# Kernel tuning notes

Measured on AMD Instinct MI355X. Metric: run time of the kernel, lower is better.

## Reference

```python
import jax, jax.numpy as jnp
import numpy as np

ROUTER_AUX_LOSS_COEF = 0.001


def setup_inputs() -> dict:
    key = jax.random.key(0)
    k1, k2, k3, k4 = jax.random.split(key, 4)
    B, S, H = 2, 2048, 2048
    E, I = 8, 768
    return {
        "hidden_states": jax.random.normal(k1, (B, S, H), dtype=jnp.float32),
        "gate_w": jax.random.normal(k2, (H, E), dtype=jnp.float32) * 0.02,
        "gate_up_proj": jax.random.normal(k3, (E, 2 * I, H), dtype=jnp.float32) * 0.02,
        "down_proj": jax.random.normal(k4, (E, H, I), dtype=jnp.float32) * 0.02,
        "num_experts_per_tok": 2,
    }


def reference(hidden_states, gate_w, gate_up_proj, down_proj, num_experts_per_tok):
    B, S, H = hidden_states.shape
    E = gate_w.shape[1]
    x = hidden_states.reshape(-1, H)  # (T, H)
    T = x.shape[0]

    # Router
    router_logits = x @ gate_w  # (T, E)
    routing_weights = jax.nn.softmax(router_logits, axis=-1)
    topk_w, selected = jax.lax.top_k(routing_weights, num_experts_per_tok)  # (T, K)
    topk_w = topk_w / jnp.sum(topk_w, axis=-1, keepdims=True)  # norm_topk_prob

    # Dense (T, E) combine weights: zero for non-selected experts. Identical math
    # to gathering per-token expert weights, but avoids materializing (T,K,2I,H).
    w_dense = jnp.zeros((T, E), x.dtype).at[jnp.arange(T)[:, None], selected].set(topk_w)

    # Expert GEMMs over all experts (non-selected contributions get weight 0)
    gate_up = jnp.einsum("th,efh->tef", x, gate_up_proj)  # (T, E, 2I)
    gate, up = jnp.split(gate_up, 2, axis=-1)
    inter = jax.nn.silu(gate) * up  # (T, E, I)
    expert_out = jnp.einsum("tei,ehi->teh", inter, down_proj)  # (T, E, H)
    final = jnp.einsum("teh,te->th", expert_out, w_dense).reshape(B, S, H)

    # Load-balancing auxiliary loss
    expert_probs = jnp.mean(routing_weights, axis=0)  # (E,)
    expert_mask = jax.nn.one_hot(selected, E, dtype=x.dtype)  # (T, K, E)
    expert_freq = jnp.mean(jnp.sum(expert_mask, axis=1), axis=0)  # (E,)
    aux_loss = jnp.sum(expert_probs * expert_freq) * E * ROUTER_AUX_LOSS_COEF

    return final, router_logits, aux_loss
```

## Files before the change

kernel.cpp:

```cpp
#include <hip/hip_runtime.h>
#include <hip/hip_bf16.h>
#include <math.h>

#define TT 4096
#define HH 2048
#define EE 8
#define II 768
#define TWOI 1536

typedef __attribute__((ext_vector_type(8))) short bf16v8;
typedef __attribute__((ext_vector_type(4))) float f32x4;

static __device__ __forceinline__ unsigned short f2bf(float f) {
    unsigned int u = __float_as_uint(f);
    unsigned int r = (u + 0x7fffu + ((u >> 16) & 1u)) >> 16;
    return (unsigned short)r;
}
static __device__ __forceinline__ float bf2f(unsigned short b) {
    return __uint_as_float(((unsigned int)b) << 16);
}
static __device__ __forceinline__ void cvt8(const float4 v0, const float4 v1,
                                            uint4& hi, uint4& lo) {
    float f[8] = {v0.x, v0.y, v0.z, v0.w, v1.x, v1.y, v1.z, v1.w};
    unsigned short h[8], l[8];
#pragma unroll
    for (int i = 0; i < 8; ++i) {
        h[i] = f2bf(f[i]);
        l[i] = f2bf(f[i] - bf2f(h[i]));
    }
    hi = make_uint4((unsigned)h[0] | ((unsigned)h[1] << 16),
                    (unsigned)h[2] | ((unsigned)h[3] << 16),
                    (unsigned)h[4] | ((unsigned)h[5] << 16),
                    (unsigned)h[6] | ((unsigned)h[7] << 16));
    lo = make_uint4((unsigned)l[0] | ((unsigned)l[1] << 16),
                    (unsigned)l[2] | ((unsigned)l[3] << 16),
                    (unsigned)l[4] | ((unsigned)l[5] << 16),
                    (unsigned)l[6] | ((unsigned)l[7] << 16));
}

__global__ __launch_bounds__(256) void router_kernel(
    const float* __restrict__ x, const float* __restrict__ gw,
    float* __restrict__ logits_out, int* __restrict__ counts,
    int* __restrict__ bucket_tok, float* __restrict__ bucket_w)
{
    const int wave = threadIdx.x >> 6;
    const int lane = threadIdx.x & 63;
    const int t = blockIdx.x * 4 + wave;

    float acc[EE];
#pragma unroll
    for (int e = 0; e < EE; ++e) acc[e] = 0.f;

    const float4* xr = (const float4*)(x + (size_t)t * HH);
    for (int i = lane; i < HH / 4; i += 64) {
        const float4 v = xr[i];
        const float* g = gw + (size_t)(i * 4) * EE;
#pragma unroll
        for (int e = 0; e < EE; ++e)
            acc[e] += v.x * g[e] + v.y * g[e + EE]
                    + v.z * g[e + 2 * EE] + v.w * g[e + 3 * EE];
    }
#pragma unroll
    for (int e = 0; e < EE; ++e) {
#pragma unroll
        for (int off = 32; off > 0; off >>= 1)
            acc[e] += __shfl_xor(acc[e], off, 64);
    }

    if (lane == 0) {
        float mx = acc[0];
#pragma unroll
        for (int e = 1; e < EE; ++e) mx = fmaxf(mx, acc[e]);
        float p[EE]; float s = 0.f;
#pragma unroll
        for (int e = 0; e < EE; ++e) { p[e] = expf(acc[e] - mx); s += p[e]; }
        const float inv = 1.f / s;
#pragma unroll
        for (int e = 0; e < EE; ++e) {
            p[e] *= inv;
            logits_out[(size_t)t * EE + e] = acc[e];
        }
        int i0 = 0;
#pragma unroll
        for (int e = 1; e < EE; ++e) if (p[e] > p[i0]) i0 = e;
        int i1 = (i0 == 0) ? 1 : 0;
#pragma unroll
        for (int e = 0; e < EE; ++e) if (e != i0 && p[e] > p[i1]) i1 = e;
        const float denom = 1.f / (p[i0] + p[i1]);
        const float w0 = p[i0] * denom, w1 = p[i1] * denom;
        int pos0 = atomicAdd(&counts[i0], 1);
        bucket_tok[i0 * TT + pos0] = t; bucket_w[i0 * TT + pos0] = w0;
        int pos1 = atomicAdd(&counts[i1], 1);
        bucket_tok[i1 * TT + pos1] = t; bucket_w[i1 * TT + pos1] = w1;
    }
}

__global__ __launch_bounds__(256) void finalize_router(
    const float* __restrict__ logits, const int* __restrict__ counts,
    int* __restrict__ offsets, float* __restrict__ aux_out)
{
    __shared__ float sums[EE];
    if (threadIdx.x < EE) sums[threadIdx.x] = 0.f;
    __syncthreads();
    float loc[EE];
#pragma unroll
    for (int e = 0; e < EE; ++e) loc[e] = 0.f;
    for (int t = threadIdx.x; t < TT; t += 256) {
        const float* lr = logits + (size_t)t * EE;
        float l[EE]; float mx = -1e30f;
#pragma unroll
        for (int e = 0; e < EE; ++e) { l[e] = lr[e]; mx = fmaxf(mx, l[e]); }
        float s = 0.f, p[EE];
#pragma unroll
        for (int e = 0; e < EE; ++e) { p[e] = expf(l[e] - mx); s += p[e]; }
        const float inv = 1.f / s;
#pragma unroll
        for (int e = 0; e < EE; ++e) loc[e] += p[e] * inv;
    }
#pragma unroll
    for (int e = 0; e < EE; ++e) atomicAdd(&sums[e], loc[e]);
    __syncthreads();
    if (threadIdx.x == 0) {
        int o = 0; float aux = 0.f;
        for (int e = 0; e < EE; ++e) {
            offsets[e] = o; o += counts[e];
            aux += (sums[e] / (float)TT) * ((float)counts[e] / (float)TT);
        }
        aux_out[0] = aux * (float)EE * 0.001f;
    }
}

#define AHI 0
#define ALO 8192
#define BHI 16384
#define BLO 24576

__global__ __launch_bounds__(256, 2) void moe_gateup(
    const float* __restrict__ x, const float* __restrict__ Wgu,
    const int* __restrict__ counts, const int* __restrict__ offsets,
    const int* __restrict__ bucket_tok, float* __restrict__ inter)
{
    const int bid = blockIdx.x;
    const int e = bid & 7;
    const int rem = bid >> 3;
    const int mb = rem / 12, nb = rem % 12;

    const int cnt = counts[e];
    const int m0 = mb * 128;
    if (m0 >= cnt) return;
    const int n0 = nb * 64;
    const int base = offsets[e];

    __shared__ unsigned char smem[32768];

    const int tid = threadIdx.x;
    const int lane = tid & 63;
    const int wid = tid >> 6;
    const int wm = wid >> 1, wn = wid & 1;

    const int srow = tid >> 1;
    const int sseg = tid & 1;
    const int arow = m0 + srow;
    const int atok = (arow < cnt) ? bucket_tok[e * TT + arow] : 0;
    const float* ag = x + (size_t)atok * HH + sseg * 16;
    const int bblk = srow >> 5, bc = srow & 31;
    const int bj = ((bblk & 1) ? II : 0) + n0 + ((bblk >> 1) << 5) + bc;
    const float* bg = Wgu + ((size_t)e * TWOI + bj) * HH + sseg * 16;
    const int au0 = srow * 64 + (((sseg << 1) | 0) ^ (srow & 3)) * 16;
    const int au1 = srow * 64 + (((sseg << 1) | 1) ^ (srow & 3)) * 16;

    int aoff[4], boff[4];
#pragma unroll
    for (int i = 0; i < 4; ++i) {
        int ra = wm * 64 + i * 16 + (lane & 15);
        aoff[i] = ra * 64 + (((lane >> 4) ^ (ra & 3)) * 16);
        int rb = wn * 64 + i * 16 + (lane & 15);
        boff[i] = rb * 64 + (((lane >> 4) ^ (rb & 3)) * 16);
    }

    f32x4 acc[4][4];
#pragma unroll
    for (int i = 0; i < 4; ++i)
#pragma unroll
        for (int j = 0; j < 4; ++j) acc[i][j] = f32x4{0.f, 0.f, 0.f, 0.f};

    float4 pa0 = *(const float4*)(ag + 0), pa1 = *(const float4*)(ag + 4);
    float4 pa2 = *(const float4*)(ag + 8), pa3 = *(const float4*)(ag + 12);
    float4 pb0 = *(const float4*)(bg + 0), pb1 = *(const float4*)(bg + 4);
    float4 pb2 = *(const float4*)(bg + 8), pb3 = *(const float4*)(bg + 12);

    const int NS = HH / 32;
    for (int s = 0; s < NS; ++s) {
        __syncthreads();
        uint4 hi, lo;
        cvt8(pa0, pa1, hi, lo);
        *(uint4*)(smem + AHI + au0) = hi; *(uint4*)(smem + ALO + au0) = lo;
        cvt8(pa2, pa3, hi, lo);
        *(uint4*)(smem + AHI + au1) = hi; *(uint4*)(smem + ALO + au1) = lo;
        cvt8(pb0, pb1, hi, lo);
        *(uint4*)(smem + BHI + au0) = hi; *(uint4*)(smem + BLO + au0) = lo;
        cvt8(pb2, pb3, hi, lo);
        *(uint4*)(smem + BHI + au1) = hi; *(uint4*)(smem + BLO + au1) = lo;
        __syncthreads();
        if (s + 1 < NS) {
            const int k0 = (s + 1) * 32;
            pa0 = *(const float4*)(ag + k0); pa1 = *(const float4*)(ag + k0 + 4);
            pa2 = *(const float4*)(ag + k0 + 8); pa3 = *(const float4*)(ag + k0 + 12);
            pb0 = *(const float4*)(bg + k0); pb1 = *(const float4*)(bg + k0 + 4);
            pb2 = *(const float4*)(bg + k0 + 8); pb3 = *(const float4*)(bg + k0 + 12);
        }
        bf16v8 ah[4], al[4], bh[4], bl[4];
#pragma unroll
        for (int i = 0; i < 4; ++i) {
            ah[i] = *(const bf16v8*)(smem + AHI + aoff[i]);
            al[i] = *(const bf16v8*)(smem + ALO + aoff[i]);
            bh[i] = *(const bf16v8*)(smem + BHI + boff[i]);
            bl[i] = *(const bf16v8*)(smem + BLO + boff[i]);
        }
#pragma unroll
        for (int i = 0; i < 4; ++i)
#pragma unroll
            for (int j = 0; j < 4; ++j) {
                acc[i][j] = __builtin_amdgcn_mfma_f32_16x16x32_bf16(ah[i], bh[j], acc[i][j], 0, 0, 0);
                acc[i][j] = __builtin_amdgcn_mfma_f32_16x16x32_bf16(ah[i], bl[j], acc[i][j], 0, 0, 0);
                acc[i][j] = __builtin_amdgcn_mfma_f32_16x16x32_bf16(al[i], bh[j], acc[i][j], 0, 0, 0);
            }
    }

#pragma unroll
    for (int mi = 0; mi < 4; ++mi)
#pragma unroll
        for (int np = 0; np < 2; ++np) {
            const f32x4 g = acc[mi][np], u = acc[mi][np + 2];
            const int colp = n0 + wn * 32 + np * 16 + (lane & 15);
#pragma unroll
            for (int j = 0; j < 4; ++j) {
                const int r = m0 + wm * 64 + mi * 16 + ((lane >> 4) << 2) + j;
                if (r < cnt) {
                    const float gg = g[j];
                    const float sv = gg / (1.f + expf(-gg));
                    inter[(size_t)(base + r) * II + colp] = sv * u[j];
                }
            }
        }
}

__global__ __launch_bounds__(256, 2) void moe_down(
    const float* __restrict__ inter, const float* __restrict__ Wd,
    const int* __restrict__ counts, const int* __restrict__ offsets,
    const int* __restrict__ bucket_tok, const float* __restrict__ bucket_w,
    float* __restrict__ out)
{
    const int bid = blockIdx.x;
    const int e = bid & 7;
    const int rem = bid >> 3;
    const int mb = rem >> 4, nb = rem & 15;

    const int cnt = counts[e];
    const int m0 = mb * 128;
    if (m0 >= cnt) return;
    const int n0 = nb * 128;
    const int base = offsets[e];

    __shared__ unsigned char smem[32768];

    const int tid = threadIdx.x;
    const int lane = tid & 63;
    const int wid = tid >> 6;
    const int wm = wid >> 1, wn = wid & 1;

    const int srow = tid >> 1;
    const int sseg = tid & 1;
    const int arow = m0 + srow;
    const int asafe = (arow < cnt) ? arow : 0;
    const float* ag = inter + (size_t)(base + asafe) * II + sseg * 16;
    const float* bg = Wd + ((size_t)e * HH + n0 + srow) * II + sseg * 16;
    const int au0 = srow * 64 + (((sseg << 1) | 0) ^ (srow & 3)) * 16;
    const int au1 = srow * 64 + (((sseg << 1) | 1) ^ (srow & 3)) * 16;

    int aoff[4], boff[4];
#pragma unroll
    for (int i = 0; i < 4; ++i) {
        int ra = wm * 64 + i * 16 + (lane & 15);
        aoff[i] = ra * 64 + (((lane >> 4) ^ (ra & 3)) * 16);
        int rb = wn * 64 + i * 16 + (lane & 15);
        boff[i] = rb * 64 + (((lane >> 4) ^ (rb & 3)) * 16);
    }

    f32x4 acc[4][4];
#pragma unroll
    for (int i = 0; i < 4; ++i)
#pragma unroll
        for (int j = 0; j < 4; ++j) acc[i][j] = f32x4{0.f, 0.f, 0.f, 0.f};

    float4 pa0 = *(const float4*)(ag + 0), pa1 = *(const float4*)(ag + 4);
    float4 pa2 = *(const float4*)(ag + 8), pa3 = *(const float4*)(ag + 12);
    float4 pb0 = *(const float4*)(bg + 0), pb1 = *(const float4*)(bg + 4);
    float4 pb2 = *(const float4*)(bg + 8), pb3 = *(const float4*)(bg + 12);

    const int NS = II / 32;
    for (int s = 0; s < NS; ++s) {
        __syncthreads();
        uint4 hi, lo;
        cvt8(pa0, pa1, hi, lo);
        *(uint4*)(smem + AHI + au0) = hi; *(uint4*)(smem + ALO + au0) = lo;
        cvt8(pa2, pa3, hi, lo);
        *(uint4*)(smem + AHI + au1) = hi; *(uint4*)(smem + ALO + au1) = lo;
        cvt8(pb0, pb1, hi, lo);
        *(uint4*)(smem + BHI + au0) = hi; *(uint4*)(smem + BLO + au0) = lo;
        cvt8(pb2, pb3, hi, lo);
        *(uint4*)(smem + BHI + au1) = hi; *(uint4*)(smem + BLO + au1) = lo;
        __syncthreads();
        if (s + 1 < NS) {
            const int k0 = (s + 1) * 32;
            pa0 = *(const float4*)(ag + k0); pa1 = *(const float4*)(ag + k0 + 4);
            pa2 = *(const float4*)(ag + k0 + 8); pa3 = *(const float4*)(ag + k0 + 12);
            pb0 = *(const float4*)(bg + k0); pb1 = *(const float4*)(bg + k0 + 4);
            pb2 = *(const float4*)(bg + k0 + 8); pb3 = *(const float4*)(bg + k0 + 12);
        }
        bf16v8 ah[4], al[4], bh[4], bl[4];
#pragma unroll
        for (int i = 0; i < 4; ++i) {
            ah[i] = *(const bf16v8*)(smem + AHI + aoff[i]);
            al[i] = *(const bf16v8*)(smem + ALO + aoff[i]);
            bh[i] = *(const bf16v8*)(smem + BHI + boff[i]);
            bl[i] = *(const bf16v8*)(smem + BLO + boff[i]);
        }
#pragma unroll
        for (int i = 0; i < 4; ++i)
#pragma unroll
            for (int j = 0; j < 4; ++j) {
                acc[i][j] = __builtin_amdgcn_mfma_f32_16x16x32_bf16(ah[i], bh[j], acc[i][j], 0, 0, 0);
                acc[i][j] = __builtin_amdgcn_mfma_f32_16x16x32_bf16(ah[i], bl[j], acc[i][j], 0, 0, 0);
                acc[i][j] = __builtin_amdgcn_mfma_f32_16x16x32_bf16(al[i], bh[j], acc[i][j], 0, 0, 0);
            }
    }

#pragma unroll
    for (int mi = 0; mi < 4; ++mi) {
        int rtok[4]; float rw[4]; int rok[4];
#pragma unroll
        for (int j = 0; j < 4; ++j) {
            const int r = m0 + wm * 64 + mi * 16 + ((lane >> 4) << 2) + j;
            rok[j] = (r < cnt);
            rtok[j] = rok[j] ? bucket_tok[e * TT + r] : 0;
            rw[j] = rok[j] ? bucket_w[e * TT + r] : 0.f;
        }
#pragma unroll
        for (int ni = 0; ni < 4; ++ni) {
            const int col = n0 + wn * 64 + ni * 16 + (lane & 15);
#pragma unroll
            for (int j = 0; j < 4; ++j)
                if (rok[j])
                    atomicAdd(out + (size_t)rtok[j] * HH + col, rw[j] * acc[mi][ni][j]);
        }
    }
}

extern "C" void kernel_launch(void* const* d_in, const int* in_sizes, int n_in,
                              void* d_out, int out_size, void* d_ws, size_t ws_size,
                              hipStream_t stream)
{
    const float* x   = (const float*)d_in[0];
    const float* gw  = (const float*)d_in[1];
    const float* wgu = (const float*)d_in[2];
    const float* wd  = (const float*)d_in[3];

    float* out_final  = (float*)d_out;
    float* out_logits = out_final + (size_t)TT * HH;
    float* out_aux    = out_logits + (size_t)TT * EE;

    int*   counts     = (int*)d_ws;
    int*   offsets    = counts + 8;
    int*   bucket_tok = (int*)d_ws + 64;
    float* bucket_w   = (float*)d_ws + 64 + EE * TT;
    float* inter      = (float*)d_ws + 64 + 2 * EE * TT;

    hipMemsetAsync(d_ws, 0, 256, stream);
    hipMemsetAsync(d_out, 0, sizeof(float) * (size_t)TT * HH, stream);

    router_kernel<<<TT / 4, 256, 0, stream>>>(x, gw, out_logits, counts,
                                              bucket_tok, bucket_w);
    finalize_router<<<1, 256, 0, stream>>>(out_logits, counts, offsets, out_aux);
    moe_gateup<<<12 * 32 * EE, 256, 0, stream>>>(x, wgu, counts, offsets,
                                                 bucket_tok, inter);
    moe_down<<<16 * 32 * EE, 256, 0, stream>>>(inter, wd, counts, offsets,
                                               bucket_tok, bucket_w, out_final);
}
```

Measured before the change: 674.6 us.

## Pre-split operands into bf16 hi/lo buffers and widen GEMM K-tiles

Adds a pre-pass that converts the expert weights to bf16 hi/lo planes, and has the router emit split activations. The GEMM kernels then load pre-split data and use a 64-wide K tile with larger shared memory, instead of converting fp32 to bf16 pairs inside every tile. The intermediate activations are also stored as hi/lo bf16. This removes redundant per-block conversion work but adds a full weight conversion pass on every call and needs a large workspace; the old path is kept as a fallback.

Measured after the change: 1.348 ms. +99.8%, slower.

```diff
diff --git a/kernel.cpp b/kernel.cpp
--- a/kernel.cpp
+++ b/kernel.cpp
@@ -38,10 +38,28 @@
                     (unsigned)l[6] | ((unsigned)l[7] << 16));
 }
 
+__global__ __launch_bounds__(256) void cvt_split(
+    const float* __restrict__ src, unsigned short* __restrict__ hi,
+    unsigned short* __restrict__ lo, int n8)
+{
+    int i = blockIdx.x * 256 + threadIdx.x;
+    const int stride = gridDim.x * 256;
+    for (; i < n8; i += stride) {
+        const float4 a = ((const float4*)src)[2 * i];
+        const float4 b = ((const float4*)src)[2 * i + 1];
+        uint4 h, l;
+        cvt8(a, b, h, l);
+        ((uint4*)hi)[i] = h;
+        ((uint4*)lo)[i] = l;
+    }
+}
+
 __global__ __launch_bounds__(256) void router_kernel(
     const float* __restrict__ x, const float* __restrict__ gw,
     float* __restrict__ logits_out, int* __restrict__ counts,
-    int* __restrict__ bucket_tok, float* __restrict__ bucket_w)
+    int* __restrict__ bucket_tok, float* __restrict__ bucket_w,
+    unsigned short* __restrict__ xhi, unsigned short* __restrict__ xlo,
+    int do_split)
 {
     const int wave = threadIdx.x >> 6;
     const int lane = threadIdx.x & 63;
@@ -59,6 +77,20 @@
         for (int e = 0; e < EE; ++e)
             acc[e] += v.x * g[e] + v.y * g[e + EE]
                     + v.z * g[e + 2 * EE] + v.w * g[e + 3 * EE];
+        if (do_split) {
+            const unsigned short h0 = f2bf(v.x), h1 = f2bf(v.y),
+                                 h2 = f2bf(v.z), h3 = f2bf(v.w);
+            const unsigned short l0 = f2bf(v.x - bf2f(h0)),
+                                 l1 = f2bf(v.y - bf2f(h1)),
+                                 l2 = f2bf(v.z - bf2f(h2)),
+                                 l3 = f2bf(v.w - bf2f(h3));
+            *(uint2*)(xhi + (size_t)t * HH + i * 4) =
+                make_uint2((unsigned)h0 | ((unsigned)h1 << 16),
+                           (unsigned)h2 | ((unsigned)h3 << 16));
+            *(uint2*)(xlo + (size_t)t * HH + i * 4) =
+                make_uint2((unsigned)l0 | ((unsigned)l1 << 16),
+                           (unsigned)l2 | ((unsigned)l3 << 16));
+        }
     }
 #pragma unroll
     for (int e = 0; e < EE; ++e) {
@@ -131,14 +163,16 @@
 }
 
 #define AHI 0
-#define ALO 8192
-#define BHI 16384
-#define BLO 24576
-
-__global__ __launch_bounds__(256, 2) void moe_gateup(
-    const float* __restrict__ x, const float* __restrict__ Wgu,
+#define ALO 16384
+#define BHI 32768
+#define BLO 49152
+
+__global__ __launch_bounds__(256, 2) void moe_gateup_v2(
+    const unsigned short* __restrict__ xhi, const unsigned short* __restrict__ xlo,
+    const unsigned short* __restrict__ guhi, const unsigned short* __restrict__ gulo,
     const int* __restrict__ counts, const int* __restrict__ offsets,
-    const int* __restrict__ bucket_tok, float* __restrict__ inter)
+    const int* __restrict__ bucket_tok,
+    unsigned short* __restrict__ ihi, unsigned short* __restrict__ ilo)
 {
     const int bid = blockIdx.x;
     const int e = bid & 7;
@@ -151,13 +185,266 @@
     const int n0 = nb * 64;
     const int base = offsets[e];
 
-    __shared__ unsigned char smem[32768];
+    __shared__ unsigned char smem[65536];
 
     const int tid = threadIdx.x;
     const int lane = tid & 63;
     const int wid = tid >> 6;
     const int wm = wid >> 1, wn = wid & 1;
 
+    const int srow = tid >> 1;
+    const int sseg = tid & 1;
+    const int arow = m0 + srow;
+    const int atok = (arow < cnt) ? bucket_tok[e * TT + arow] : 0;
+    const size_t aoffg = (size_t)atok * HH + sseg * 32;
+    const int bblk = srow >> 5, bc = srow & 31;
+    const int bj = ((bblk & 1) ? II : 0) + n0 + ((bblk >> 1) << 5) + bc;
+    const size_t boffg = ((size_t)e * TWOI + bj) * HH + sseg * 32;
+
+    int wu[4];
+#pragma unroll
+    for (int j = 0; j < 4; ++j)
+        wu[j] = srow * 128 + ((((sseg << 2) | j) ^ (srow & 7)) << 4);
+
+    int aoff[2][4], boff[2][4];
+#pragma unroll
+    for (int ks = 0; ks < 2; ++ks)
+#pragma unroll
+        for (int i = 0; i < 4; ++i) {
+            const int ra = wm * 64 + i * 16 + (lane & 15);
+            aoff[ks][i] = ra * 128 + ((((ks << 2) | (lane >> 4)) ^ (ra & 7)) << 4);
+            const int rb = wn * 64 + i * 16 + (lane & 15);
+            boff[ks][i] = rb * 128 + ((((ks << 2) | (lane >> 4)) ^ (rb & 7)) << 4);
+        }
+
+    f32x4 acc[4][4];
+#pragma unroll
+    for (int i = 0; i < 4; ++i)
+#pragma unroll
+        for (int j = 0; j < 4; ++j) acc[i][j] = f32x4{0.f, 0.f, 0.f, 0.f};
+
+    uint4 pAh[4], pAl[4], pBh[4], pBl[4];
+#pragma unroll
+    for (int j = 0; j < 4; ++j) {
+        pAh[j] = *(const uint4*)(xhi + aoffg + j * 8);
+        pAl[j] = *(const uint4*)(xlo + aoffg + j * 8);
+        pBh[j] = *(const uint4*)(guhi + boffg + j * 8);
+        pBl[j] = *(const uint4*)(gulo + boffg + j * 8);
+    }
+
+    const int NS = HH / 64;
+    for (int s = 0; s < NS; ++s) {
+        __syncthreads();
+#pragma unroll
+        for (int j = 0; j < 4; ++j) {
+            *(uint4*)(smem + AHI + wu[j]) = pAh[j];
+            *(uint4*)(smem + ALO + wu[j]) = pAl[j];
+            *(uint4*)(smem + BHI + wu[j]) = pBh[j];
+            *(uint4*)(smem + BLO + wu[j]) = pBl[j];
+        }
+        __syncthreads();
+        if (s + 1 < NS) {
+            const int k0 = (s + 1) * 64;
+#pragma unroll
+            for (int j = 0; j < 4; ++j) {
+                pAh[j] = *(const uint4*)(xhi + aoffg + k0 + j * 8);
+                pAl[j] = *(const uint4*)(xlo + aoffg + k0 + j * 8);
+                pBh[j] = *(const uint4*)(guhi + boffg + k0 + j * 8);
+                pBl[j] = *(const uint4*)(gulo + boffg + k0 + j * 8);
+            }
+        }
+#pragma unroll
+        for (int ks = 0; ks < 2; ++ks) {
+            bf16v8 ah[4], al[4], bh[4], bl[4];
+#pragma unroll
+            for (int i = 0; i < 4; ++i) {
+                ah[i] = *(const bf16v8*)(smem + AHI + aoff[ks][i]);
+                al[i] = *(const bf16v8*)(smem + ALO + aoff[ks][i]);
+                bh[i] = *(const bf16v8*)(smem + BHI + boff[ks][i]);
+                bl[i] = *(const bf16v8*)(smem + BLO + boff[ks][i]);
+            }
+#pragma unroll
+            for (int i = 0; i < 4; ++i)
+#pragma unroll
+                for (int j = 0; j < 4; ++j) {
+                    acc[i][j] = __builtin_amdgcn_mfma_f32_16x16x32_bf16(ah[i], bh[j], acc[i][j], 0, 0, 0);
+                    acc[i][j] = __builtin_amdgcn_mfma_f32_16x16x32_bf16(ah[i], bl[j], acc[i][j], 0, 0, 0);
+                    acc[i][j] = __builtin_amdgcn_mfma_f32_16x16x32_bf16(al[i], bh[j], acc[i][j], 0, 0, 0);
+                }
+        }
+    }
+
+#pragma unroll
+    for (int mi = 0; mi < 4; ++mi)
+#pragma unroll
+        for (int np = 0; np < 2; ++np) {
+            const f32x4 g = acc[mi][np], u = acc[mi][np + 2];
+            const int colp = n0 + wn * 32 + np * 16 + (lane & 15);
+#pragma unroll
+            for (int j = 0; j < 4; ++j) {
+                const int r = m0 + wm * 64 + mi * 16 + ((lane >> 4) << 2) + j;
+                if (r < cnt) {
+                    const float gg = g[j];
+                    const float val = gg / (1.f + expf(-gg)) * u[j];
+                    const unsigned short h = f2bf(val);
+                    const unsigned short l = f2bf(val - bf2f(h));
+                    ihi[(size_t)(base + r) * II + colp] = h;
+                    ilo[(size_t)(base + r) * II + colp] = l;
+                }
+            }
+        }
+}
+
+__global__ __launch_bounds__(256, 2) void moe_down_v2(
+    const unsigned short* __restrict__ ihi, const unsigned short* __restrict__ ilo,
+    const unsigned short* __restrict__ wdhi, const unsigned short* __restrict__ wdlo,
+    const int* __restrict__ counts, const int* __restrict__ offsets,
+    const int* __restrict__ bucket_tok, const float* __restrict__ bucket_w,
+    float* __restrict__ out)
+{
+    const int bid = blockIdx.x;
+    const int e = bid & 7;
+    const int rem = bid >> 3;
+    const int mb = rem >> 4, nb = rem & 15;
+
+    const int cnt = counts[e];
+    const int m0 = mb * 128;
+    if (m0 >= cnt) return;
+    const int n0 = nb * 128;
+    const int base = offsets[e];
+
+    __shared__ unsigned char smem[65536];
+
+    const int tid = threadIdx.x;
+    const int lane = tid & 63;
+    const int wid = tid >> 6;
+    const int wm = wid >> 1, wn = wid & 1;
+
+    const int srow = tid >> 1;
+    const int sseg = tid & 1;
+    const int arow = m0 + srow;
+    const int asafe = (arow < cnt) ? arow : 0;
+    const size_t aoffg = (size_t)(base + asafe) * II + sseg * 32;
+    const size_t boffg = ((size_t)e * HH + n0 + srow) * II + sseg * 32;
+
+    int wu[4];
+#pragma unroll
+    for (int j = 0; j < 4; ++j)
+        wu[j] = srow * 128 + ((((sseg << 2) | j) ^ (srow & 7)) << 4);
+
+    int aoff[2][4], boff[2][4];
+#pragma unroll
+    for (int ks = 0; ks < 2; ++ks)
+#pragma unroll
+        for (int i = 0; i < 4; ++i) {
+            const int ra = wm * 64 + i * 16 + (lane & 15);
+            aoff[ks][i] = ra * 128 + ((((ks << 2) | (lane >> 4)) ^ (ra & 7)) << 4);
+            const int rb = wn * 64 + i * 16 + (lane & 15);
+            boff[ks][i] = rb * 128 + ((((ks << 2) | (lane >> 4)) ^ (rb & 7)) << 4);
+        }
+
+    f32x4 acc[4][4];
+#pragma unroll
+    for (int i = 0; i < 4; ++i)
+#pragma unroll
+        for (int j = 0; j < 4; ++j) acc[i][j] = f32x4{0.f, 0.f, 0.f, 0.f};
+
+    uint4 pAh[4], pAl[4], pBh[4], pBl[4];
+#pragma unroll
+    for (int j = 0; j < 4; ++j) {
+        pAh[j] = *(const uint4*)(ihi + aoffg + j * 8);
+        pAl[j] = *(const uint4*)(ilo + aoffg + j * 8);
+        pBh[j] = *(const uint4*)(wdhi + boffg + j * 8);
+        pBl[j] = *(const uint4*)(wdlo + boffg + j * 8);
+    }
+
+    const int NS = II / 64;
+    for (int s = 0; s < NS; ++s) {
+        __syncthreads();
+#pragma unroll
+        for (int j = 0; j < 4; ++j) {
+            *(uint4*)(smem + AHI + wu[j]) = pAh[j];
+            *(uint4*)(smem + ALO + wu[j]) = pAl[j];
+            *(uint4*)(smem + BHI + wu[j]) = pBh[j];
+            *(uint4*)(smem + BLO + wu[j]) = pBl[j];
+        }
+        __syncthreads();
+        if (s + 1 < NS) {
+            const int k0 = (s + 1) * 64;
+#pragma unroll
+            for (int j = 0; j < 4; ++j) {
+                pAh[j] = *(const uint4*)(ihi + aoffg + k0 + j * 8);
+                pAl[j] = *(const uint4*)(ilo + aoffg + k0 + j * 8);
+                pBh[j] = *(const uint4*)(wdhi + boffg + k0 + j * 8);
+                pBl[j] = *(const uint4*)(wdlo + boffg + k0 + j * 8);
+            }
+        }
+#pragma unroll
+        for (int ks = 0; ks < 2; ++ks) {
+            bf16v8 ah[4], al[4], bh[4], bl[4];
+#pragma unroll
+            for (int i = 0; i < 4; ++i) {
+                ah[i] = *(const bf16v8*)(smem + AHI + aoff[ks][i]);
+                al[i] = *(const bf16v8*)(smem + ALO + aoff[ks][i]);
+                bh[i] = *(const bf16v8*)(smem + BHI + boff[ks][i]);
+                bl[i] = *(const bf16v8*)(smem + BLO + boff[ks][i]);
+            }
+#pragma unroll
+            for (int i = 0; i < 4; ++i)
+#pragma unroll
+                for (int j = 0; j < 4; ++j) {
+                    acc[i][j] = __builtin_amdgcn_mfma_f32_16x16x32_bf16(ah[i], bh[j], acc[i][j], 0, 0, 0);
+                    acc[i][j] = __builtin_amdgcn_mfma_f32_16x16x32_bf16(ah[i], bl[j], acc[i][j], 0, 0, 0);
+                    acc[i][j] = __builtin_amdgcn_mfma_f32_16x16x32_bf16(al[i], bh[j], acc[i][j], 0, 0, 0);
+                }
+        }
+    }
+
+#pragma unroll
+    for (int mi = 0; mi < 4; ++mi) {
+        int rtok[4]; float rw[4]; int rok[4];
+#pragma unroll
+        for (int j = 0; j < 4; ++j) {
+            const int r = m0 + wm * 64 + mi * 16 + ((lane >> 4) << 2) + j;
+            rok[j] = (r < cnt);
+            rtok[j] = rok[j] ? bucket_tok[e * TT + r] : 0;
+            rw[j] = rok[j] ? bucket_w[e * TT + r] : 0.f;
+        }
+#pragma unroll
+        for (int ni = 0; ni < 4; ++ni) {
+            const int col = n0 + wn * 64 + ni * 16 + (lane & 15);
+#pragma unroll
+            for (int j = 0; j < 4; ++j)
+                if (rok[j])
+                    atomicAdd(out + (size_t)rtok[j] * HH + col, rw[j] * acc[mi][ni][j]);
+        }
+    }
+}
+
+#define AHI1 0
+#define ALO1 8192
+#define BHI1 16384
+#define BLO1 24576
+
+__global__ __launch_bounds__(256, 2) void moe_gateup_r4(
+    const float* __restrict__ x, const float* __restrict__ Wgu,
+    const int* __restrict__ counts, const int* __restrict__ offsets,
+    const int* __restrict__ bucket_tok, float* __restrict__ inter)
+{
+    const int bid = blockIdx.x;
+    const int e = bid & 7;
+    const int rem = bid >> 3;
+    const int mb = rem / 12, nb = rem % 12;
+    const int cnt = counts[e];
+    const int m0 = mb * 128;
+    if (m0 >= cnt) return;
+    const int n0 = nb * 64;
+    const int base = offsets[e];
+    __shared__ unsigned char smem[32768];
+    const int tid = threadIdx.x;
+    const int lane = tid & 63;
+    const int wid = tid >> 6;
+    const int wm = wid >> 1, wn = wid & 1;
     const int srow = tid >> 1;
     const int sseg = tid & 1;
     const int arow = m0 + srow;
@@ -168,7 +455,6 @@
     const float* bg = Wgu + ((size_t)e * TWOI + bj) * HH + sseg * 16;
     const int au0 = srow * 64 + (((sseg << 1) | 0) ^ (srow & 3)) * 16;
     const int au1 = srow * 64 + (((sseg << 1) | 1) ^ (srow & 3)) * 16;
-
     int aoff[4], boff[4];
 #pragma unroll
     for (int i = 0; i < 4; ++i) {
@@ -177,30 +463,27 @@
         int rb = wn * 64 + i * 16 + (lane & 15);
         boff[i] = rb * 64 + (((lane >> 4) ^ (rb & 3)) * 16);
     }
-
     f32x4 acc[4][4];
 #pragma unroll
     for (int i = 0; i < 4; ++i)
 #pragma unroll
         for (int j = 0; j < 4; ++j) acc[i][j] = f32x4{0.f, 0.f, 0.f, 0.f};
-
     float4 pa0 = *(const float4*)(ag + 0), pa1 = *(const float4*)(ag + 4);
     float4 pa2 = *(const float4*)(ag + 8), pa3 = *(const float4*)(ag + 12);
     float4 pb0 = *(const float4*)(bg + 0), pb1 = *(const float4*)(bg + 4);
     float4 pb2 = *(const float4*)(bg + 8), pb3 = *(const float4*)(bg + 12);
-
     const int NS = HH / 32;
     for (int s = 0; s < NS; ++s) {
         __syncthreads();
         uint4 hi, lo;
         cvt8(pa0, pa1, hi, lo);
-        *(uint4*)(smem + AHI + au0) = hi; *(uint4*)(smem + ALO + au0) = lo;
+        *(uint4*)(smem + AHI1 + au0) = hi; *(uint4*)(smem + ALO1 + au0) = lo;
         cvt8(pa2, pa3, hi, lo);
-        *(uint4*)(smem + AHI + au1) = hi; *(uint4*)(smem + ALO + au1) = lo;
+        *(uint4*)(smem + AHI1 + au1) = hi; *(uint4*)(smem + ALO1 + au1) = lo;
         cvt8(pb0, pb1, hi, lo);
-        *(uint4*)(smem + BHI + au0) = hi; *(uint4*)(smem + BLO + au0) = lo;
+        *(uint4*)(smem + BHI1 + au0) = hi; *(uint4*)(smem + BLO1 + au0) = lo;
         cvt8(pb2, pb3, hi, lo);
-        *(uint4*)(smem + BHI + au1) = hi; *(uint4*)(smem + BLO + au1) = lo;
+        *(uint4*)(smem + BHI1 + au1) = hi; *(uint4*)(smem + BLO1 + au1) = lo;
         __syncthreads();
         if (s + 1 < NS) {
             const int k0 = (s + 1) * 32;
@@ -212,10 +495,10 @@
         bf16v8 ah[4], al[4], bh[4], bl[4];
 #pragma unroll
         for (int i = 0; i < 4; ++i) {
-            ah[i] = *(const bf16v8*)(smem + AHI + aoff[i]);
-            al[i] = *(const bf16v8*)(smem + ALO + aoff[i]);
-            bh[i] = *(const bf16v8*)(smem + BHI + boff[i]);
-            bl[i] = *(const bf16v8*)(smem + BLO + boff[i]);
+            ah[i] = *(const bf16v8*)(smem + AHI1 + aoff[i]);
+            al[i] = *(const bf16v8*)(smem + ALO1 + aoff[i]);
+            bh[i] = *(const bf16v8*)(smem + BHI1 + boff[i]);
+            bl[i] = *(const bf16v8*)(smem + BLO1 + boff[i]);
         }
 #pragma unroll
         for (int i = 0; i < 4; ++i)
@@ -226,7 +509,6 @@
                 acc[i][j] = __builtin_amdgcn_mfma_f32_16x16x32_bf16(al[i], bh[j], acc[i][j], 0, 0, 0);
             }
     }
-
 #pragma unroll
     for (int mi = 0; mi < 4; ++mi)
 #pragma unroll
@@ -238,14 +520,13 @@
                 const int r = m0 + wm * 64 + mi * 16 + ((lane >> 4) << 2) + j;
                 if (r < cnt) {
                     const float gg = g[j];
-                    const float sv = gg / (1.f + expf(-gg));
-                    inter[(size_t)(base + r) * II + colp] = sv * u[j];
+                    inter[(size_t)(base + r) * II + colp] = gg / (1.f + expf(-gg)) * u[j];
                 }
             }
         }
 }
 
-__global__ __launch_bounds__(256, 2) void moe_down(
+__global__ __launch_bounds__(256, 2) void moe_down_r4(
     const float* __restrict__ inter, const float* __restrict__ Wd,
     const int* __restrict__ counts, const int* __restrict__ offsets,
     const int* __restrict__ bucket_tok, const float* __restrict__ bucket_w,
@@ -255,20 +536,16 @@
     const int e = bid & 7;
     const int rem = bid >> 3;
     const int mb = rem >> 4, nb = rem & 15;
-
     const int cnt = counts[e];
     const int m0 = mb * 128;
     if (m0 >= cnt) return;
     const int n0 = nb * 128;
     const int base = offsets[e];
-
     __shared__ unsigned char smem[32768];
-
     const int tid = threadIdx.x;
     const int lane = tid & 63;
     const int wid = tid >> 6;
     const int wm = wid >> 1, wn = wid & 1;
-
     const int srow = tid >> 1;
     const int sseg = tid & 1;
     const int arow = m0 + srow;
@@ -277,7 +554,6 @@
     const float* bg = Wd + ((size_t)e * HH + n0 + srow) * II + sseg * 16;
     const int au0 = srow * 64 + (((sseg << 1) | 0) ^ (srow & 3)) * 16;
     const int au1 = srow * 64 + (((sseg << 1) | 1) ^ (srow & 3)) * 16;
-
     int aoff[4], boff[4];
 #pragma unroll
     for (int i = 0; i < 4; ++i) {
@@ -286,30 +562,27 @@
         int rb = wn * 64 + i * 16 + (lane & 15);
         boff[i] = rb * 64 + (((lane >> 4) ^ (rb & 3)) * 16);
     }
-
     f32x4 acc[4][4];
 #pragma unroll
     for (int i = 0; i < 4; ++i)
 #pragma unroll
         for (int j = 0; j < 4; ++j) acc[i][j] = f32x4{0.f, 0.f, 0.f, 0.f};
-
     float4 pa0 = *(const float4*)(ag + 0), pa1 = *(const float4*)(ag + 4);
     float4 pa2 = *(const float4*)(ag + 8), pa3 = *(const float4*)(ag + 12);
     float4 pb0 = *(const float4*)(bg + 0), pb1 = *(const float4*)(bg + 4);
     float4 pb2 = *(const float4*)(bg + 8), pb3 = *(const float4*)(bg + 12);
-
     const int NS = II / 32;
     for (int s = 0; s < NS; ++s) {
         __syncthreads();
         uint4 hi, lo;
         cvt8(pa0, pa1, hi, lo);
-        *(uint4*)(smem + AHI + au0) = hi; *(uint4*)(smem + ALO + au0) = lo;
+        *(uint4*)(smem + AHI1 + au0) = hi; *(uint4*)(smem + ALO1 + au0) = lo;
         cvt8(pa2, pa3, hi, lo);
-        *(uint4*)(smem + AHI + au1) = hi; *(uint4*)(smem + ALO + au1) = lo;
+        *(uint4*)(smem + AHI1 + au1) = hi; *(uint4*)(smem + ALO1 + au1) = lo;
         cvt8(pb0, pb1, hi, lo);
-        *(uint4*)(smem + BHI + au0) = hi; *(uint4*)(smem + BLO + au0) = lo;
+        *(uint4*)(smem + BHI1 + au0) = hi; *(uint4*)(smem + BLO1 + au0) = lo;
         cvt8(pb2, pb3, hi, lo);
-        *(uint4*)(smem + BHI + au1) = hi; *(uint4*)(smem + BLO + au1) = lo;
+        *(uint4*)(smem + BHI1 + au1) = hi; *(uint4*)(smem + BLO1 + au1) = lo;
         __syncthreads();
         if (s + 1 < NS) {
             const int k0 = (s + 1) * 32;
@@ -321,10 +594,10 @@
         bf16v8 ah[4], al[4], bh[4], bl[4];
 #pragma unroll
         for (int i = 0; i < 4; ++i) {
-            ah[i] = *(const bf16v8*)(smem + AHI + aoff[i]);
-            al[i] = *(const bf16v8*)(smem + ALO + aoff[i]);
-            bh[i] = *(const bf16v8*)(smem + BHI + boff[i]);
-            bl[i] = *(const bf16v8*)(smem + BLO + boff[i]);
+            ah[i] = *(const bf16v8*)(smem + AHI1 + aoff[i]);
+            al[i] = *(const bf16v8*)(smem + ALO1 + aoff[i]);
+            bh[i] = *(const bf16v8*)(smem + BHI1 + boff[i]);
+            bl[i] = *(const bf16v8*)(smem + BLO1 + boff[i]);
         }
 #pragma unroll
         for (int i = 0; i < 4; ++i)
@@ -335,7 +608,6 @@
                 acc[i][j] = __builtin_amdgcn_mfma_f32_16x16x32_bf16(al[i], bh[j], acc[i][j], 0, 0, 0);
             }
     }
-
 #pragma unroll
     for (int mi = 0; mi < 4; ++mi) {
         int rtok[4]; float rw[4]; int rok[4];
@@ -374,16 +646,47 @@
     int*   offsets    = counts + 8;
     int*   bucket_tok = (int*)d_ws + 64;
     float* bucket_w   = (float*)d_ws + 64 + EE * TT;
-    float* inter      = (float*)d_ws + 64 + 2 * EE * TT;
+
+    const size_t HDR   = 262400;
+    const size_t SZ_X  = (size_t)TT * HH * 2;
+    const size_t SZ_GU = (size_t)EE * TWOI * HH * 2;
+    const size_t SZ_WD = (size_t)EE * HH * II * 2;
+    const size_t SZ_I  = (size_t)2 * TT * II * 2;
+    const size_t need = HDR + 2 * (SZ_X + SZ_GU + SZ_WD + SZ_I);
 
     hipMemsetAsync(d_ws, 0, 256, stream);
     hipMemsetAsync(d_out, 0, sizeof(float) * (size_t)TT * HH, stream);
 
-    router_kernel<<<TT / 4, 256, 0, stream>>>(x, gw, out_logits, counts,
-                                              bucket_tok, bucket_w);
-    finalize_router<<<1, 256, 0, stream>>>(out_logits, counts, offsets, out_aux);
-    moe_gateup<<<12 * 32 * EE, 256, 0, stream>>>(x, wgu, counts, offsets,
-                                                 bucket_tok, inter);
-    moe_down<<<16 * 32 * EE, 256, 0, stream>>>(inter, wd, counts, offsets,
-                                               bucket_tok, bucket_w, out_final);
-}
+    if (ws_size >= need) {
+        unsigned char* p = (unsigned char*)d_ws + HDR;
+        unsigned short* xhi  = (unsigned short*)p;            p += SZ_X;
+        unsigned short* xlo  = (unsigned short*)p;            p += SZ_X;
+        unsigned short* guhi = (unsigned short*)p;            p += SZ_GU;
+        unsigned short* gulo = (unsigned short*)p;            p += SZ_GU;
+        unsigned short* wdhi = (unsigned short*)p;            p += SZ_WD;
+        unsigned short* wdlo = (unsigned short*)p;            p += SZ_WD;
+        unsigned short* ihi  = (unsigned short*)p;            p += SZ_I;
+        unsigned short* ilo  = (unsigned short*)p;
+
+        cvt_split<<<2048, 256, 0, stream>>>(wgu, guhi, gulo, EE * TWOI * HH / 8);
+        cvt_split<<<2048, 256, 0, stream>>>(wd, wdhi, wdlo, EE * HH * II / 8);
+        router_kernel<<<TT / 4, 256, 0, stream>>>(x, gw, out_logits, counts,
+                                                  bucket_tok, bucket_w, xhi, xlo, 1);
+        finalize_router<<<1, 256, 0, stream>>>(out_logits, counts, offsets, out_aux);
+        moe_gateup_v2<<<12 * 32 * EE, 256, 0, stream>>>(
+            xhi, xlo, guhi, gulo, counts, offsets, bucket_tok, ihi, ilo);
+        moe_down_v2<<<16 * 32 * EE, 256, 0, stream>>>(
+            ihi, ilo, wdhi, wdlo, counts, offsets, bucket_tok, bucket_w, out_final);
+    } else {
+        float* inter = (float*)d_ws + 64 + 2 * EE * TT;
+        router_kernel<<<TT / 4, 256, 0, stream>>>(x, gw, out_logits, counts,
+                                                  bucket_tok, bucket_w,
+                                                  (unsigned short*)counts,
+                                                  (unsigned short*)counts, 0);
+        finalize_router<<<1, 256, 0, stream>>>(out_logits, counts, offsets, out_aux);
+        moe_gateup_r4<<<12 * 32 * EE, 256, 0, stream>>>(x, wgu, counts, offsets,
+                                                        bucket_tok, inter);
+        moe_down_r4<<<16 * 32 * EE, 256, 0, stream>>>(inter, wd, counts, offsets,
+                                                      bucket_tok, bucket_w, out_final);
+    }
+}
```
